# Kernel optimization log

Hardware: AMD Instinct MI355X
Metric: run time of the kernel (lower is better)

## Reference

```python
import jax, jax.numpy as jnp
import numpy as np

EPS = 1e-10
REG = 1e-6  # regularization_weight passed to sparse_image_warp


def _phi(r2):
    # order-2 polyharmonic (thin-plate) kernel: 0.5 * r^2 * log(r^2)
    return 0.5 * r2 * jnp.log(jnp.maximum(r2, EPS))


def _tps_interpolate(train_pts, train_vals, query_pts, reg):
    # train_pts: (B,N,2), train_vals: (B,N,2), query_pts: (B,Q,2)
    b, n, _ = train_pts.shape
    d2 = jnp.sum((train_pts[:, :, None, :] - train_pts[:, None, :, :]) ** 2, -1)
    A = _phi(d2) + reg * jnp.eye(n, dtype=train_pts.dtype)  # (B,N,N)
    ones_n = jnp.ones((b, n, 1), train_pts.dtype)
    Bm = jnp.concatenate([train_pts, ones_n], -1)  # (B,N,3)
    top = jnp.concatenate([A, Bm], -1)
    bot = jnp.concatenate([jnp.swapaxes(Bm, 1, 2), jnp.zeros((b, 3, 3), train_pts.dtype)], -1)
    lhs = jnp.concatenate([top, bot], 1)  # (B,N+3,N+3)
    rhs = jnp.concatenate([train_vals, jnp.zeros((b, 3, train_vals.shape[-1]), train_vals.dtype)], 1)
    sol = jnp.linalg.solve(lhs, rhs)
    w, v = sol[:, :n], sol[:, n:]  # rbf weights (B,N,2), affine (B,3,2)
    q2 = jnp.sum((query_pts[:, :, None, :] - train_pts[:, None, :, :]) ** 2, -1)  # (B,Q,N)
    rbf = jnp.einsum('bqn,bnd->bqd', _phi(q2), w)
    ones_q = jnp.ones((b, query_pts.shape[1], 1), query_pts.dtype)
    lin = jnp.einsum('bqk,bkd->bqd', jnp.concatenate([query_pts, ones_q], -1), v)
    return rbf + lin


def _bilinear_sample(image, qy, qx):
    # image: (B,H,W,C); qy,qx: (B,Q) float query coordinates (TF dense_image_warp clamping)
    B, H, W, C = image.shape
    y0 = jnp.clip(jnp.floor(qy), 0, H - 2).astype(jnp.int32)
    x0 = jnp.clip(jnp.floor(qx), 0, W - 2).astype(jnp.int32)
    ay = jnp.clip(qy - y0.astype(qy.dtype), 0.0, 1.0)[..., None]
    ax = jnp.clip(qx - x0.astype(qx.dtype), 0.0, 1.0)[..., None]
    bi = jnp.arange(B)[:, None]
    g = lambda yi, xi: image[bi, yi, xi]  # gather -> (B,Q,C)
    top = g(y0, x0) * (1 - ax) + g(y0, x0 + 1) * ax
    bot = g(y0 + 1, x0) * (1 - ax) + g(y0 + 1, x0 + 1) * ax
    return top * (1 - ay) + bot * ay


def _sparse_image_warp(image, src, dst, reg):
    # TF semantics: flows at control points = dst - src, interpolated at dst; sample at grid - flow
    B, H, W, C = image.shape
    flows_ctrl = dst - src  # (B,N,2)
    gy, gx = jnp.meshgrid(jnp.arange(H, dtype=image.dtype), jnp.arange(W, dtype=image.dtype), indexing='ij')
    grid = jnp.broadcast_to(jnp.stack([gy, gx], -1).reshape(1, H * W, 2), (B, H * W, 2))
    dense_flow = _tps_interpolate(dst, flows_ctrl, grid, reg)  # (B,HW,2)
    query = grid - dense_flow
    warped = _bilinear_sample(image, query[..., 0], query[..., 1])
    return warped.reshape(B, H, W, C), dense_flow.reshape(B, H, W, 2)


def setup_inputs() -> dict:
    key = jax.random.key(0)
    ks = jax.random.split(key, 8)
    B, C, H, W = 16, 64, 112, 112
    n_ldmark = 16
    F = C * H * W
    x = jax.random.normal(ks[0], (B, C, H, W), jnp.float32)
    images_rendered = jax.random.normal(ks[1], (B, H, W, C), jnp.float32)
    scales = jax.random.uniform(ks[2], (B, 1), jnp.float32)
    W1 = jax.random.normal(ks[3], (128, F), jnp.float32) / np.float32(np.sqrt(F))
    b1 = jnp.zeros((128,), jnp.float32)
    W2 = jax.random.normal(ks[4], (n_ldmark * 2, 128), jnp.float32) / np.float32(np.sqrt(128))
    b2 = jnp.zeros((n_ldmark * 2,), jnp.float32)
    W3 = jax.random.normal(ks[5], (n_ldmark * 2, 128), jnp.float32) / np.float32(np.sqrt(128))
    b3 = jnp.zeros((n_ldmark * 2,), jnp.float32)
    # torch.normal(mean=0, std=50, size=(n_ldmark,2)) + [0.5*H, 0.5*W], fixed for determinism
    landmarks_mean = jax.random.normal(ks[6], (n_ldmark, 2), jnp.float32) * 50.0 \
        + jnp.array([0.5 * H, 0.5 * W], jnp.float32)
    return {"x": x, "images_rendered": images_rendered, "scales": scales,
            "W1": W1, "b1": b1, "W2": W2, "b2": b2, "W3": W3, "b3": b3,
            "landmarks_mean": landmarks_mean}


def reference(x, images_rendered, scales, W1, b1, W2, b2, W3, b3, landmarks_mean):
    B = x.shape[0]
    n_ldmark = landmarks_mean.shape[0]
    feat = x.reshape(B, -1)
    out = feat @ W1.T + b1  # (B,128)
    landmarks_pred = out @ W2.T + b2 + landmarks_mean.reshape(-1)  # (B, 2*n_ldmark)
    landmarks_disp = (out @ W3.T + b3) * scales
    # original uses .detach().clone() on landmark coords -> stop_gradient
    src = jax.lax.stop_gradient(landmarks_pred).reshape(B, n_ldmark, 2)
    dst = jax.lax.stop_gradient(landmarks_pred + landmarks_disp).reshape(B, n_ldmark, 2)
    # torch.norm(..., dim=(1,2)) = per-batch Frobenius norm, then mean
    landmarks_norm = jnp.mean(jnp.sqrt(jnp.sum((src - dst) ** 2, axis=(1, 2))))
    warped, _dense_flow = _sparse_image_warp(images_rendered, src, dst, REG)
    images_transformed = jnp.transpose(warped, (0, 3, 1, 2))  # NHWC -> NCHW
    return images_transformed, landmarks_pred, landmarks_norm
```

## Files before the change

kernel.cpp:

```cpp
#include <hip/hip_runtime.h>
#include <math.h>

#define F_K 802816
#define KC 1024
#define NB1 784
#define NIMG 12845056
#define PRED_OFF 12845056
#define NORM_OFF 12845568

__global__ __launch_bounds__(256) void k_gemm1(const float* __restrict__ x,
                                               const float* __restrict__ w1,
                                               float* __restrict__ part) {
  __shared__ float xs[16][64];
  __shared__ float wt[64][128];
  const int t = threadIdx.x;
  const int blk = blockIdx.x;
  const int k0 = blk * KC;
  const int nq = t & 31, bp = t >> 5;
  const int b0 = bp * 2, n0 = nq * 4;
  float4 acc0 = {0.f,0.f,0.f,0.f}, acc1 = {0.f,0.f,0.f,0.f};

  const int xb = t >> 4, xko = (t & 15) * 4;
  const int wn = t >> 1, wkb = (t & 1) * 32;
  const float* xrow = x  + (size_t)xb * F_K + k0 + xko;
  const float* wrow = w1 + (size_t)wn * F_K + k0 + wkb;

  for (int kt = 0; kt < KC / 64; ++kt) {
    float4 xv = *reinterpret_cast<const float4*>(xrow + kt * 64);
    *reinterpret_cast<float4*>(&xs[xb][xko]) = xv;
#pragma unroll
    for (int j = 0; j < 8; ++j) {
      float4 wv = *reinterpret_cast<const float4*>(wrow + kt * 64 + 4 * j);
      int kk = wkb + 4 * j;
      wt[kk + 0][wn] = wv.x; wt[kk + 1][wn] = wv.y;
      wt[kk + 2][wn] = wv.z; wt[kk + 3][wn] = wv.w;
    }
    __syncthreads();
    const float4* xa4 = reinterpret_cast<const float4*>(&xs[b0][0]);
    const float4* xb4 = reinterpret_cast<const float4*>(&xs[b0 + 1][0]);
#pragma unroll
    for (int kk4 = 0; kk4 < 16; ++kk4) {
      float4 xa = xa4[kk4], xbv = xb4[kk4];
      float xaf[4] = {xa.x, xa.y, xa.z, xa.w};
      float xbf[4] = {xbv.x, xbv.y, xbv.z, xbv.w};
#pragma unroll
      for (int j = 0; j < 4; ++j) {
        float4 wv = *reinterpret_cast<const float4*>(&wt[kk4 * 4 + j][n0]);
        acc0.x += xaf[j] * wv.x; acc0.y += xaf[j] * wv.y;
        acc0.z += xaf[j] * wv.z; acc0.w += xaf[j] * wv.w;
        acc1.x += xbf[j] * wv.x; acc1.y += xbf[j] * wv.y;
        acc1.z += xbf[j] * wv.z; acc1.w += xbf[j] * wv.w;
      }
    }
    __syncthreads();
  }
  float* pp = part + (size_t)blk * 2048;
  *reinterpret_cast<float4*>(pp + b0 * 128 + n0) = acc0;
  *reinterpret_cast<float4*>(pp + (b0 + 1) * 128 + n0) = acc1;
}

__global__ __launch_bounds__(256) void k_red(const float* __restrict__ part,
                                             float* __restrict__ p2) {
  int pc = blockIdx.x >> 3, ib = blockIdx.x & 7;
  int idx = ib * 256 + threadIdx.x;
  const float* p = part + (size_t)pc * 49 * 2048 + idx;
  float s = 0.f;
  for (int q = 0; q < 49; ++q) s += p[(size_t)q * 2048];
  p2[pc * 2048 + idx] = s;
}

__global__ __launch_bounds__(64) void k_small(const float* __restrict__ p2,
    const float* __restrict__ b1, const float* __restrict__ W2, const float* __restrict__ b2,
    const float* __restrict__ W3, const float* __restrict__ b3,
    const float* __restrict__ lmean, const float* __restrict__ scales,
    float* __restrict__ dout_pred, float* __restrict__ coef, float* __restrict__ norms) {
  const int b = blockIdx.x, lane = threadIdx.x;
  __shared__ float o[128], dflat[32], fl[32], A[19][22], farr[19], sol[19][2];

  for (int h = 0; h < 2; ++h) {
    int n = lane + 64 * h;
    float s = b1[n];
    for (int pc = 0; pc < 16; ++pc) s += p2[pc * 2048 + b * 128 + n];
    o[n] = s;
  }
  __syncthreads();

  const int j = lane & 31;
  const float* Wm = (lane < 32) ? (W2 + j * 128) : (W3 + j * 128);
  float acc = 0.f;
#pragma unroll 4
  for (int n = 0; n < 128; ++n) acc += o[n] * Wm[n];
  float other = __shfl(acc, j + 32);
  float sc = scales[b];
  float dspv = 0.f;
  if (lane < 32) {
    float predv = acc + b2[j] + lmean[j];
    dspv = (other + b3[j]) * sc;
    dout_pred[b * 32 + j] = predv;
    dflat[j] = predv + dspv;
    fl[j] = dspv;
  }
  float s2 = (lane < 32) ? dspv * dspv : 0.f;
  for (int off = 32; off; off >>= 1) s2 += __shfl_xor(s2, off);
  if (lane == 0) norms[b] = sqrtf(s2);
  __syncthreads();

  for (int cell = lane; cell < 19 * 21; cell += 64) {
    int r = cell / 21, c = cell - (cell / 21) * 21;
    float v;
    if (r < 16) {
      if (c < 16) {
        float dy = dflat[2*r] - dflat[2*c], dx = dflat[2*r+1] - dflat[2*c+1];
        float d2 = dy * dy + dx * dx;
        v = 0.5f * d2 * logf(fmaxf(d2, 1e-10f));
        if (r == c) v += 1e-6f;
      } else if (c == 16) v = dflat[2*r];
      else if (c == 17) v = dflat[2*r+1];
      else if (c == 18) v = 1.0f;
      else if (c == 19) v = fl[2*r];
      else               v = fl[2*r+1];
    } else {
      int rr = r - 16;
      if (c < 16) v = (rr == 0) ? dflat[2*c] : (rr == 1) ? dflat[2*c+1] : 1.0f;
      else        v = 0.0f;
    }
    A[r][c] = v;
  }
  __syncthreads();

  for (int k = 0; k < 19; ++k) {
    float av = (lane >= k && lane < 19) ? fabsf(A[lane][k]) : -1.0f;
    int idx = lane;
    for (int off = 32; off; off >>= 1) {
      float v2 = __shfl_xor(av, off);
      int  i2 = __shfl_xor(idx, off);
      if (v2 > av) { av = v2; idx = i2; }
    }
    idx = __shfl(idx, 0);
    if (idx != k && lane < 21) {
      float tmp = A[k][lane]; A[k][lane] = A[idx][lane]; A[idx][lane] = tmp;
    }
    __syncthreads();
    float invp = 1.0f / A[k][k];
    if (lane < 19) farr[lane] = (lane > k) ? A[lane][k] * invp : 0.0f;
    __syncthreads();
    int nr = 18 - k, nc = 20 - k;
    for (int cell = lane; cell < nr * nc; cell += 64) {
      int i = k + 1 + cell / nc, jj = k + 1 + cell % nc;
      A[i][jj] -= farr[i] * A[k][jj];
    }
    __syncthreads();
  }
  for (int k = 18; k >= 0; --k) {
    if (lane < 2) sol[k][lane] = A[k][19 + lane] / A[k][k];
    __syncthreads();
    if (lane < 2 * k) {
      int i = lane >> 1, c = lane & 1;
      A[i][19 + c] -= A[i][k] * sol[k][c];
    }
    __syncthreads();
  }
  float* cf = coef + b * 80;
  if (lane < 32) { cf[lane] = sol[lane >> 1][lane & 1]; cf[38 + lane] = dflat[lane]; }
  else if (lane < 38) cf[lane] = sol[16 + ((lane - 32) >> 1)][(lane - 32) & 1];
}

__global__ __launch_bounds__(256) void k_warp(const float* __restrict__ img,
                                              const float* __restrict__ coef,
                                              const float* __restrict__ norms,
                                              float* __restrict__ out) {
  const int bid = blockIdx.x;
  const int b = bid / 112, y = bid - (bid / 112) * 112;
  const int t = threadIdx.x;
  __shared__ float qy[112], qx[112];
  __shared__ float cw[32], cv[6], cd[32];
  __shared__ float tile[64][113];

  if (bid == 0 && t == 0) {
    float s = 0.f;
    for (int i = 0; i < 16; ++i) s += norms[i];
    out[NORM_OFF] = s * (1.0f / 16.0f);
  }
  const float* cf = coef + b * 80;
  if (t < 70) {
    float v = cf[t];
    if (t < 32) cw[t] = v;
    else if (t < 38) cv[t - 32] = v;
    else cd[t - 38] = v;
  }
  __syncthreads();

  if (t < 112) {
    float fy = (float)y, fx = (float)t;
    float s0 = cv[0] * fy + cv[2] * fx + cv[4];
    float s1 = cv[1] * fy + cv[3] * fx + cv[5];
#pragma unroll
    for (int i = 0; i < 16; ++i) {
      float dy = fy - cd[2 * i], dx = fx - cd[2 * i + 1];
      float d2 = dy * dy + dx * dx;
      float ph = 0.5f * d2 * logf(fmaxf(d2, 1e-10f));
      s0 += ph * cw[2 * i];
      s1 += ph * cw[2 * i + 1];
    }
    qy[t] = fy - s0;
    qx[t] = fx - s1;
  }
  __syncthreads();

  const int wave = t >> 6, lane = t & 63;
  for (int p = 0; p < 28; ++p) {
    int xx = wave * 28 + p;
    float fy = qy[xx], fx = qx[xx];
    float y0f = fminf(fmaxf(floorf(fy), 0.f), 110.f);
    float x0f = fminf(fmaxf(floorf(fx), 0.f), 110.f);
    float ay = fminf(fmaxf(fy - y0f, 0.f), 1.f);
    float ax = fminf(fmaxf(fx - x0f, 0.f), 1.f);
    int y0 = (int)y0f, x0 = (int)x0f;
    const float* p00 = img + (((size_t)(b * 112 + y0) * 112 + x0) * 64) + lane;
    float v00 = p00[0], v01 = p00[64];
    float v10 = p00[112 * 64], v11 = p00[112 * 64 + 64];
    float top = v00 * (1.f - ax) + v01 * ax;
    float bot = v10 * (1.f - ax) + v11 * ax;
    tile[lane][xx] = top * (1.f - ay) + bot * ay;
  }
  __syncthreads();

  float* ob = out + (size_t)b * 64 * 12544 + y * 112;
  for (int i = 0; i < 28; ++i) {
    int idx = i * 256 + t;
    int c = idx / 112, xx = idx - c * 112;
    ob[(size_t)c * 12544 + xx] = tile[c][xx];
  }
}

extern "C" void kernel_launch(void* const* d_in, const int* in_sizes, int n_in,
                              void* d_out, int out_size, void* d_ws, size_t ws_size,
                              hipStream_t stream) {
  const float* x      = (const float*)d_in[0];
  const float* img    = (const float*)d_in[1];
  const float* scales = (const float*)d_in[2];
  const float* W1     = (const float*)d_in[3];
  const float* b1     = (const float*)d_in[4];
  const float* W2     = (const float*)d_in[5];
  const float* b2     = (const float*)d_in[6];
  const float* W3     = (const float*)d_in[7];
  const float* b3     = (const float*)d_in[8];
  const float* lmean  = (const float*)d_in[9];
  float* out = (float*)d_out;
  float* ws  = (float*)d_ws;

  float* P1   = ws;
  float* P2   = P1 + (size_t)NB1 * 2048;
  float* COEF = P2 + 16 * 2048;
  float* NORM = COEF + 16 * 80;

  k_gemm1<<<NB1, 256, 0, stream>>>(x, W1, P1);
  k_red  <<<128, 256, 0, stream>>>(P1, P2);
  k_small<<<16, 64, 0, stream>>>(P2, b1, W2, b2, W3, b3, lmean, scales,
                                 out + PRED_OFF, COEF, NORM);
  k_warp <<<16 * 112, 256, 0, stream>>>(img, COEF, NORM, out);
}
```

Before: 202.6 us.

## Load GEMM tiles directly to LDS with swizzle and split-K across waves

The first-layer GEMM kernel now uses global_load_lds to move 16-byte chunks of x and W1 straight into shared memory. An XOR swizzle on the W1 layout avoids bank conflicts, replacing the old register-staged transposed scalar stores. Each wave handles a quarter of the K tile with a 4x8 register accumulator block, and the four waves' partial sums are reduced through shared memory at the end. The bilinear sampling loop also gets an unroll-4 pragma. This adds an extra LDS reduction step and depends on the builtin being available; otherwise it falls back to a plain copy.

```diff
diff --git a/kernel.cpp b/kernel.cpp
--- a/kernel.cpp
+++ b/kernel.cpp
@@ -1,62 +1,103 @@
 #include <hip/hip_runtime.h>
 #include <math.h>
+#include <stdint.h>
 
 #define F_K 802816
 #define KC 1024
 #define NB1 784
-#define NIMG 12845056
 #define PRED_OFF 12845056
 #define NORM_OFF 12845568
+
+#define AS3 __attribute__((address_space(3)))
+#define AS1 __attribute__((address_space(1)))
+
+__device__ __forceinline__ void gload16(const float* gsrc, float* ldsbase) {
+#if __has_builtin(__builtin_amdgcn_global_load_lds)
+  __builtin_amdgcn_global_load_lds((const AS1 uint32_t*)gsrc, (AS3 uint32_t*)ldsbase, 16, 0, 0);
+#else
+  int lane = threadIdx.x & 63;
+  *reinterpret_cast<float4*>(ldsbase + lane * 4) = *reinterpret_cast<const float4*>(gsrc);
+#endif
+}
 
 __global__ __launch_bounds__(256) void k_gemm1(const float* __restrict__ x,
                                                const float* __restrict__ w1,
                                                float* __restrict__ part) {
-  __shared__ float xs[16][64];
-  __shared__ float wt[64][128];
+  __shared__ __align__(16) float xs[16 * 64];
+  __shared__ __align__(16) float ws[128 * 64];
   const int t = threadIdx.x;
-  const int blk = blockIdx.x;
-  const int k0 = blk * KC;
-  const int nq = t & 31, bp = t >> 5;
-  const int b0 = bp * 2, n0 = nq * 4;
-  float4 acc0 = {0.f,0.f,0.f,0.f}, acc1 = {0.f,0.f,0.f,0.f};
-
-  const int xb = t >> 4, xko = (t & 15) * 4;
-  const int wn = t >> 1, wkb = (t & 1) * 32;
-  const float* xrow = x  + (size_t)xb * F_K + k0 + xko;
-  const float* wrow = w1 + (size_t)wn * F_K + k0 + wkb;
+  const int wave = t >> 6, lane = t & 63;
+  const int nl = t & 15;
+  const int bg = (t >> 4) & 3;
+  const size_t k0 = (size_t)blockIdx.x * KC;
+
+  const int xf = wave * 64 + lane;
+  const float* xsrc = x + (size_t)(xf >> 4) * F_K + k0 + 4 * (xf & 15);
+  float* xdst = xs + wave * 256;
+
+  const float* wsrc[8];
+#pragma unroll
+  for (int cc = 0; cc < 8; ++cc) {
+    int f = (wave * 8 + cc) * 64 + lane;
+    int n = f >> 4, c = f & 15;
+    int sc = c ^ (n & 7);
+    wsrc[cc] = w1 + (size_t)n * F_K + k0 + 4 * sc;
+  }
+  float* wbase = ws + wave * 2048;
+
+  float acc[4][8];
+#pragma unroll
+  for (int i = 0; i < 4; ++i)
+#pragma unroll
+    for (int j = 0; j < 8; ++j) acc[i][j] = 0.f;
 
   for (int kt = 0; kt < KC / 64; ++kt) {
-    float4 xv = *reinterpret_cast<const float4*>(xrow + kt * 64);
-    *reinterpret_cast<float4*>(&xs[xb][xko]) = xv;
-#pragma unroll
-    for (int j = 0; j < 8; ++j) {
-      float4 wv = *reinterpret_cast<const float4*>(wrow + kt * 64 + 4 * j);
-      int kk = wkb + 4 * j;
-      wt[kk + 0][wn] = wv.x; wt[kk + 1][wn] = wv.y;
-      wt[kk + 2][wn] = wv.z; wt[kk + 3][wn] = wv.w;
-    }
-    __syncthreads();
-    const float4* xa4 = reinterpret_cast<const float4*>(&xs[b0][0]);
-    const float4* xb4 = reinterpret_cast<const float4*>(&xs[b0 + 1][0]);
-#pragma unroll
-    for (int kk4 = 0; kk4 < 16; ++kk4) {
-      float4 xa = xa4[kk4], xbv = xb4[kk4];
-      float xaf[4] = {xa.x, xa.y, xa.z, xa.w};
-      float xbf[4] = {xbv.x, xbv.y, xbv.z, xbv.w};
-#pragma unroll
-      for (int j = 0; j < 4; ++j) {
-        float4 wv = *reinterpret_cast<const float4*>(&wt[kk4 * 4 + j][n0]);
-        acc0.x += xaf[j] * wv.x; acc0.y += xaf[j] * wv.y;
-        acc0.z += xaf[j] * wv.z; acc0.w += xaf[j] * wv.w;
-        acc1.x += xbf[j] * wv.x; acc1.y += xbf[j] * wv.y;
-        acc1.z += xbf[j] * wv.z; acc1.w += xbf[j] * wv.w;
+    gload16(xsrc + kt * 64, xdst);
+#pragma unroll
+    for (int cc = 0; cc < 8; ++cc) gload16(wsrc[cc] + kt * 64, wbase + cc * 256);
+    __syncthreads();
+#pragma unroll
+    for (int q = 0; q < 4; ++q) {
+      const int kk4 = 4 * wave + q;
+      float4 xv[4];
+#pragma unroll
+      for (int i = 0; i < 4; ++i)
+        xv[i] = *reinterpret_cast<const float4*>(&xs[(4 * bg + i) * 64 + 4 * kk4]);
+      const int c = kk4 ^ (nl & 7);
+#pragma unroll
+      for (int j = 0; j < 8; ++j) {
+        float4 wv = *reinterpret_cast<const float4*>(&ws[(16 * j + nl) * 64 + 4 * c]);
+#pragma unroll
+        for (int i = 0; i < 4; ++i) {
+          acc[i][j] += xv[i].x * wv.x;
+          acc[i][j] += xv[i].y * wv.y;
+          acc[i][j] += xv[i].z * wv.z;
+          acc[i][j] += xv[i].w * wv.w;
+        }
       }
     }
     __syncthreads();
   }
-  float* pp = part + (size_t)blk * 2048;
-  *reinterpret_cast<float4*>(pp + b0 * 128 + n0) = acc0;
-  *reinterpret_cast<float4*>(pp + (b0 + 1) * 128 + n0) = acc1;
+
+  float* red = ws;
+#pragma unroll
+  for (int i = 0; i < 4; ++i)
+#pragma unroll
+    for (int j = 0; j < 8; ++j)
+      red[wave * 2048 + (4 * bg + i) * 128 + 16 * j + nl] = acc[i][j];
+  __syncthreads();
+  const int o8 = t * 8;
+  float4 s0 = {0, 0, 0, 0}, s1 = {0, 0, 0, 0};
+#pragma unroll
+  for (int w = 0; w < 4; ++w) {
+    float4 a = *reinterpret_cast<const float4*>(&red[w * 2048 + o8]);
+    float4 b = *reinterpret_cast<const float4*>(&red[w * 2048 + o8 + 4]);
+    s0.x += a.x; s0.y += a.y; s0.z += a.z; s0.w += a.w;
+    s1.x += b.x; s1.y += b.y; s1.z += b.z; s1.w += b.w;
+  }
+  float* pp = part + (size_t)blockIdx.x * 2048 + o8;
+  *reinterpret_cast<float4*>(pp) = s0;
+  *reinterpret_cast<float4*>(pp + 4) = s1;
 }
 
 __global__ __launch_bounds__(256) void k_red(const float* __restrict__ part,
@@ -208,6 +249,7 @@
   __syncthreads();
 
   const int wave = t >> 6, lane = t & 63;
+#pragma unroll 4
   for (int p = 0; p < 28; ++p) {
     int xx = wave * 28 + p;
     float fy = qy[xx], fx = qx[xx];
```

Measured after the change: 184.1 us. 1.1x faster.

## Restructure GEMM1 as split-K over output slices with direct-to-LDS X loads

Applied to the files above, without the earlier changes.

Rewrites the large feature GEMM so each block owns 8 output columns over a K-slice. W1 is streamed straight into registers with double-buffered float4 loads, and x is staged via global_load_lds with explicit waitcnt scheduling. Partial sums are reduced with wave shuffles and LDS across waves, and the reduction kernel now sums 56 slices. The aim is to stream the W1 matrix (the dominant traffic) closer to peak bandwidth with an XCD-aware block mapping. This trades that for high register pressure from 64 accumulators and hand-written waitcnt correctness risk.

```diff
diff --git a/kernel.cpp b/kernel.cpp
--- a/kernel.cpp
+++ b/kernel.cpp
@@ -1,72 +1,130 @@
 #include <hip/hip_runtime.h>
 #include <math.h>
+#include <stdint.h>
 
 #define F_K 802816
-#define KC 1024
-#define NB1 784
-#define NIMG 12845056
+#define NSL 56
+#define KSL 14336
+#define NTL 28
+#define KT  512
 #define PRED_OFF 12845056
 #define NORM_OFF 12845568
 
-__global__ __launch_bounds__(256) void k_gemm1(const float* __restrict__ x,
-                                               const float* __restrict__ w1,
-                                               float* __restrict__ part) {
-  __shared__ float xs[16][64];
-  __shared__ float wt[64][128];
+#define AS3 __attribute__((address_space(3)))
+#define AS1 __attribute__((address_space(1)))
+
+__device__ __forceinline__ void gload16(const float* gsrc, float* ldsbase) {
+  __builtin_amdgcn_global_load_lds((const AS1 uint32_t*)gsrc, (AS3 uint32_t*)ldsbase, 16, 0, 0);
+}
+
+__global__ __launch_bounds__(256, 4) void k_gemm1(const float* __restrict__ x,
+                                                  const float* __restrict__ w1,
+                                                  float* __restrict__ part) {
+  __shared__ __align__(16) float xs[4 * 2048];
   const int t = threadIdx.x;
-  const int blk = blockIdx.x;
-  const int k0 = blk * KC;
-  const int nq = t & 31, bp = t >> 5;
-  const int b0 = bp * 2, n0 = nq * 4;
-  float4 acc0 = {0.f,0.f,0.f,0.f}, acc1 = {0.f,0.f,0.f,0.f};
-
-  const int xb = t >> 4, xko = (t & 15) * 4;
-  const int wn = t >> 1, wkb = (t & 1) * 32;
-  const float* xrow = x  + (size_t)xb * F_K + k0 + xko;
-  const float* wrow = w1 + (size_t)wn * F_K + k0 + wkb;
-
-  for (int kt = 0; kt < KC / 64; ++kt) {
-    float4 xv = *reinterpret_cast<const float4*>(xrow + kt * 64);
-    *reinterpret_cast<float4*>(&xs[xb][xko]) = xv;
-#pragma unroll
-    for (int j = 0; j < 8; ++j) {
-      float4 wv = *reinterpret_cast<const float4*>(wrow + kt * 64 + 4 * j);
-      int kk = wkb + 4 * j;
-      wt[kk + 0][wn] = wv.x; wt[kk + 1][wn] = wv.y;
-      wt[kk + 2][wn] = wv.z; wt[kk + 3][wn] = wv.w;
-    }
-    __syncthreads();
-    const float4* xa4 = reinterpret_cast<const float4*>(&xs[b0][0]);
-    const float4* xb4 = reinterpret_cast<const float4*>(&xs[b0 + 1][0]);
-#pragma unroll
-    for (int kk4 = 0; kk4 < 16; ++kk4) {
-      float4 xa = xa4[kk4], xbv = xb4[kk4];
-      float xaf[4] = {xa.x, xa.y, xa.z, xa.w};
-      float xbf[4] = {xbv.x, xbv.y, xbv.z, xbv.w};
-#pragma unroll
-      for (int j = 0; j < 4; ++j) {
-        float4 wv = *reinterpret_cast<const float4*>(&wt[kk4 * 4 + j][n0]);
-        acc0.x += xaf[j] * wv.x; acc0.y += xaf[j] * wv.y;
-        acc0.z += xaf[j] * wv.z; acc0.w += xaf[j] * wv.w;
-        acc1.x += xbf[j] * wv.x; acc1.y += xbf[j] * wv.y;
-        acc1.z += xbf[j] * wv.z; acc1.w += xbf[j] * wv.w;
-      }
-    }
-    __syncthreads();
-  }
-  float* pp = part + (size_t)blk * 2048;
-  *reinterpret_cast<float4*>(pp + b0 * 128 + n0) = acc0;
-  *reinterpret_cast<float4*>(pp + (b0 + 1) * 128 + n0) = acc1;
+  const int wave = t >> 6, lane = t & 63;
+  const int hi = lane >> 5, kx = lane & 31;
+  const int bid = blockIdx.x;
+  const int xcd = bid & 7, j = bid >> 3;
+  const int p = j & 15, s = xcd + 8 * (j >> 4);
+
+  const size_t kb0 = (size_t)s * KSL + 128 * wave + 4 * kx;
+  const float* wptr = w1 + (size_t)(8 * p + hi) * F_K + kb0;
+  const float* xptr = x + (size_t)hi * F_K + kb0;
+  float* xw = xs + wave * 2048;
+
+  float acc[16][4];
+#pragma unroll
+  for (int b = 0; b < 16; ++b)
+#pragma unroll
+    for (int c = 0; c < 4; ++c) acc[b][c] = 0.f;
+
+#define STAGE_X()                                                     \
+  {                                                                   \
+    _Pragma("unroll") for (int cc = 0; cc < 8; ++cc)                  \
+        gload16(xptr + (size_t)(2 * cc) * F_K, xw + cc * 256);        \
+  }
+#define LOADW(dst, OFF)                                               \
+  {                                                                   \
+    _Pragma("unroll") for (int c = 0; c < 4; ++c)                     \
+        dst[c] = *reinterpret_cast<const float4*>(                    \
+            wptr + (size_t)(2 * c) * F_K + (OFF));                    \
+  }
+#define COMP(WREG)                                                    \
+  {                                                                   \
+    _Pragma("unroll") for (int b = 0; b < 16; ++b) {                  \
+      float4 xv = *reinterpret_cast<const float4*>(&xw[b * 128 + 4 * kx]); \
+      _Pragma("unroll") for (int c = 0; c < 4; ++c) {                 \
+        acc[b][c] += WREG[c].x * xv.x; acc[b][c] += WREG[c].y * xv.y; \
+        acc[b][c] += WREG[c].z * xv.z; acc[b][c] += WREG[c].w * xv.w; \
+      }                                                               \
+    }                                                                 \
+  }
+
+  float4 wA[4], wB[4];
+  STAGE_X();
+  LOADW(wA, 0);
+
+  for (int kt = 0; kt < NTL; kt += 2) {
+    LOADW(wB, KT);
+    asm volatile("s_waitcnt vmcnt(4)" ::: "memory");
+    __builtin_amdgcn_sched_barrier(0);
+    COMP(wA);
+    __builtin_amdgcn_sched_barrier(0);
+    asm volatile("s_waitcnt lgkmcnt(0)" ::: "memory");
+    __builtin_amdgcn_sched_barrier(0);
+    wptr += KT; xptr += KT;
+    STAGE_X();
+    if (kt + 2 < NTL) {
+      LOADW(wA, KT);
+      asm volatile("s_waitcnt vmcnt(4)" ::: "memory");
+    } else {
+      asm volatile("s_waitcnt vmcnt(0)" ::: "memory");
+    }
+    __builtin_amdgcn_sched_barrier(0);
+    COMP(wB);
+    __builtin_amdgcn_sched_barrier(0);
+    asm volatile("s_waitcnt lgkmcnt(0)" ::: "memory");
+    __builtin_amdgcn_sched_barrier(0);
+    wptr += KT; xptr += KT;
+    if (kt + 2 < NTL) STAGE_X();
+  }
+#undef STAGE_X
+#undef LOADW
+#undef COMP
+
+#pragma unroll
+  for (int b = 0; b < 16; ++b)
+#pragma unroll
+    for (int c = 0; c < 4; ++c) {
+      float v = acc[b][c];
+      v += __shfl_xor(v, 1);
+      v += __shfl_xor(v, 2);
+      v += __shfl_xor(v, 4);
+      v += __shfl_xor(v, 8);
+      v += __shfl_xor(v, 16);
+      acc[b][c] = v;
+    }
+  if (kx < 16) {
+#pragma unroll
+    for (int c = 0; c < 4; ++c)
+      xs[wave * 2048 + kx * 8 + 2 * c + hi] = acc[kx][c];
+  }
+  __syncthreads();
+  if (t < 128) {
+    float v = xs[t] + xs[2048 + t] + xs[4096 + t] + xs[6144 + t];
+    part[(size_t)s * 2048 + (size_t)(t >> 3) * 128 + 8 * p + (t & 7)] = v;
+  }
 }
 
 __global__ __launch_bounds__(256) void k_red(const float* __restrict__ part,
                                              float* __restrict__ p2) {
-  int pc = blockIdx.x >> 3, ib = blockIdx.x & 7;
-  int idx = ib * 256 + threadIdx.x;
-  const float* p = part + (size_t)pc * 49 * 2048 + idx;
-  float s = 0.f;
-  for (int q = 0; q < 49; ++q) s += p[(size_t)q * 2048];
-  p2[pc * 2048 + idx] = s;
+  int idx = blockIdx.x * 256 + threadIdx.x;
+  const float* p = part + idx;
+  float ssum = 0.f;
+#pragma unroll 8
+  for (int s = 0; s < NSL; ++s) ssum += p[(size_t)s * 2048];
+  p2[idx] = ssum;
 }
 
 __global__ __launch_bounds__(64) void k_small(const float* __restrict__ p2,
@@ -77,12 +135,8 @@
   const int b = blockIdx.x, lane = threadIdx.x;
   __shared__ float o[128], dflat[32], fl[32], A[19][22], farr[19], sol[19][2];
 
-  for (int h = 0; h < 2; ++h) {
-    int n = lane + 64 * h;
-    float s = b1[n];
-    for (int pc = 0; pc < 16; ++pc) s += p2[pc * 2048 + b * 128 + n];
-    o[n] = s;
-  }
+  o[lane]      = p2[b * 128 + lane]      + b1[lane];
+  o[lane + 64] = p2[b * 128 + 64 + lane] + b1[64 + lane];
   __syncthreads();
 
   const int j = lane & 31;
@@ -208,6 +262,7 @@
   __syncthreads();
 
   const int wave = t >> 6, lane = t & 63;
+#pragma unroll 4
   for (int p = 0; p < 28; ++p) {
     int xx = wave * 28 + p;
     float fy = qy[xx], fx = qx[xx];
@@ -250,12 +305,12 @@
   float* ws  = (float*)d_ws;
 
   float* P1   = ws;
-  float* P2   = P1 + (size_t)NB1 * 2048;
-  float* COEF = P2 + 16 * 2048;
+  float* P2   = P1 + (size_t)NSL * 2048;
+  float* COEF = P2 + 2048;
   float* NORM = COEF + 16 * 80;
 
-  k_gemm1<<<NB1, 256, 0, stream>>>(x, W1, P1);
-  k_red  <<<128, 256, 0, stream>>>(P1, P2);
+  k_gemm1<<<NSL * 16, 256, 0, stream>>>(x, W1, P1);
+  k_red  <<<8, 256, 0, stream>>>(P1, P2);
   k_small<<<16, 64, 0, stream>>>(P2, b1, W2, b2, W3, b3, lmean, scales,
                                  out + PRED_OFF, COEF, NORM);
   k_warp <<<16 * 112, 256, 0, stream>>>(img, COEF, NORM, out);
```

New measurement: 539.9 us. +166.5%, slower.
